# Optimization experiments

Hardware: AMD Instinct MI355X
Metric: run time of the kernel (lower is better)

## Reference

```python
import jax, jax.numpy as jnp
import numpy as np
from jax import lax

MIN_VALUE = 0.0
MAX_VALUE = 1.0

# 5-point Laplacian stencil kernel, OIHW layout
_LAP_KERNEL = jnp.array([[0.0, 1.0, 0.0],
                         [1.0, -4.0, 1.0],
                         [0.0, 1.0, 0.0]], dtype=jnp.float32).reshape(1, 1, 3, 3)


def _laplacian(u):
    # u: [B, 1, H, W], zero-padded 3x3 stencil (SAME)
    return lax.conv_general_dilated(
        u, _LAP_KERNEL, window_strides=(1, 1), padding='SAME',
        dimension_numbers=('NCHW', 'OIHW', 'NCHW'))


def _step(u, params):
    # Fisher-Kolmogorov reaction-diffusion step:
    #   diff = D * laplacian(u) + rho * u * (1 - u)
    D = params[:, 0:1]    # [B,1,H,W]
    rho = params[:, 1:2]  # [B,1,H,W]
    return D * _laplacian(u) + rho * u * (1.0 - u)


def setup_inputs() -> dict:
    key = jax.random.key(0)
    k1, k2, k3 = jax.random.split(key, 3)
    B, H, W = 32, 256, 256
    u = jax.random.uniform(k1, (B, 1, H, W), dtype=jnp.float32)
    params = jax.random.uniform(k2, (B, 2, H, W), dtype=jnp.float32)
    t = jax.random.randint(k3, (B,), 0, 32, dtype=jnp.int32)
    return {"u": u, "params": params, "t": t}


def reference(u, params, t):
    # Original: for step in range(max(t)): u[t>step] += step(u[t>step], params[t>step]); clip(u).
    # The step is per-sample local, so masked gather/scatter == predicated full update.
    max_duration = int(jnp.max(t))  # static trip count

    def body(step, u):
        mask = (t > step).astype(u.dtype)[:, None, None, None]  # [B,1,1,1]
        u = u + mask * _step(u, params)
        return jnp.clip(u, MIN_VALUE, MAX_VALUE)

    return lax.fori_loop(0, max_duration, body, u)
```

## Files before the change

kernel.cpp:

```cpp
#include <hip/hip_runtime.h>

#define HH 256
#define WW 256
#define PLANE (HH * WW)
#define CORE 16
#define HALO 16
#define SLAB 48
#define NW 16
#define RPW 3

__device__ __forceinline__ float dpp_shfl_up1(float x) {
    return __int_as_float(__builtin_amdgcn_update_dpp(
        0, __float_as_int(x), 0x138 , 0xf, 0xf, true));
}
__device__ __forceinline__ float dpp_shfl_dn1(float x) {
    return __int_as_float(__builtin_amdgcn_update_dpp(
        0, __float_as_int(x), 0x130 , 0xf, 0xf, true));
}

__global__ __launch_bounds__(1024, 8)
void rd_occ_kernel(const float* __restrict__ uin,
                   const float* __restrict__ params,
                   const int* __restrict__ t,
                   float* __restrict__ uout,
                   int base, int k)
{
    __shared__ float4 vt[2][NW][64];
    __shared__ float4 vb[2][NW][64];

    const int blk   = blockIdx.x;
    const int b     = blk >> 4;
    const int strip = blk & 15;
    const int r0    = strip * CORE;
    const int w     = threadIdx.x >> 6;
    const int lane  = threadIdx.x & 63;
    const int c0    = lane << 2;

    int ls = t[b] - base;
    ls = ls < 0 ? 0 : (ls > k ? k : ls);

    const int top_gap = HALO - (RPW * w + RPW - 1);
    const int bot_gap = RPW * w - (HALO + CORE - 1);
    int d_min = top_gap > bot_gap ? top_gap : bot_gap;
    if (d_min < 0) d_min = 0;
    int my_steps = ls - d_min;
    if (my_steps < 0) my_steps = 0;

    const int growbase = r0 - HALO + RPW * w;
    const size_t ubase = (size_t)b * PLANE;
    const size_t pbase = (size_t)b * 2 * PLANE;

    float u[RPW][4], pD[RPW][4], pR[RPW][4];

    #pragma unroll
    for (int dr = 0; dr < RPW; ++dr) {
        const int grow = growbase + dr;
        const bool inimg = (grow >= 0) && (grow < HH);
        int dist = 0;
        if (grow < r0)                 dist = r0 - grow;
        else if (grow > r0 + CORE - 1) dist = grow - (r0 + CORE - 1);
        const bool needU = inimg && (dist <= ls);
        const bool needP = inimg && (dist < ls);

        if (needU) {
            const float4 uu = *reinterpret_cast<const float4*>(uin + ubase + (size_t)grow * WW + c0);
            u[dr][0] = uu.x; u[dr][1] = uu.y; u[dr][2] = uu.z; u[dr][3] = uu.w;
        } else {
            u[dr][0] = u[dr][1] = u[dr][2] = u[dr][3] = 0.f;
        }
        if (needP) {
            const float4 dd = *reinterpret_cast<const float4*>(params + pbase + (size_t)grow * WW + c0);
            const float4 rr = *reinterpret_cast<const float4*>(params + pbase + PLANE + (size_t)grow * WW + c0);
            pD[dr][0] = dd.x; pD[dr][1] = dd.y; pD[dr][2] = dd.z; pD[dr][3] = dd.w;
            pR[dr][0] = rr.x; pR[dr][1] = rr.y; pR[dr][2] = rr.z; pR[dr][3] = rr.w;
        } else {
            pD[dr][0] = pD[dr][1] = pD[dr][2] = pD[dr][3] = 0.f;
            pR[dr][0] = pR[dr][1] = pR[dr][2] = pR[dr][3] = 0.f;
        }
    }

    if (ls > 0) {
        vt[0][w][lane] = make_float4(u[0][0], u[0][1], u[0][2], u[0][3]);
        vb[0][w][lane] = make_float4(u[RPW-1][0], u[RPW-1][1], u[RPW-1][2], u[RPW-1][3]);

        for (int s = 0; s < ls; ++s) {
            __syncthreads();
            if (s < my_steps) {
                const int cur = s & 1;

                float upr[4] = {0.f, 0.f, 0.f, 0.f};
                float dnr[4] = {0.f, 0.f, 0.f, 0.f};
                if (w > 0)      { float4 v = vb[cur][w-1][lane]; upr[0]=v.x; upr[1]=v.y; upr[2]=v.z; upr[3]=v.w; }
                if (w < NW - 1) { float4 v = vt[cur][w+1][lane]; dnr[0]=v.x; dnr[1]=v.y; dnr[2]=v.z; dnr[3]=v.w; }

                float up_old[4];
                #pragma unroll
                for (int dr = 0; dr < RPW; ++dr) {
                    const float lf = dpp_shfl_up1(u[dr][3]);
                    const float rt = dpp_shfl_dn1(u[dr][0]);

                    float old[4], un[4];
                    #pragma unroll
                    for (int c = 0; c < 4; ++c) old[c] = u[dr][c];

                    #pragma unroll
                    for (int c = 0; c < 4; ++c) {
                        const float upv = dr ? up_old[c] : upr[c];
                        const float dnv = (dr < RPW - 1) ? u[dr+1][c] : dnr[c];
                        const float lv  = c ? old[c-1] : lf;
                        const float rv  = (c < 3) ? old[c+1] : rt;
                        const float uc  = old[c];
                        const float s4  = (upv + dnv) + (lv + rv);
                        const float lap = fmaf(-4.0f, uc, s4);
                        const float g   = fmaf(-uc, uc, uc);
                        const float a   = fmaf(pD[dr][c], lap, uc);
                        const float nv  = fmaf(pR[dr][c], g, a);
                        un[c] = __builtin_amdgcn_fmed3f(nv, 0.0f, 1.0f);
                    }
                    #pragma unroll
                    for (int c = 0; c < 4; ++c) { u[dr][c] = un[c]; up_old[c] = old[c]; }
                }

                const int nxt = cur ^ 1;
                vt[nxt][w][lane] = make_float4(u[0][0], u[0][1], u[0][2], u[0][3]);
                vb[nxt][w][lane] = make_float4(u[RPW-1][0], u[RPW-1][1], u[RPW-1][2], u[RPW-1][3]);
            }
        }
    }

    #pragma unroll
    for (int dr = 0; dr < RPW; ++dr) {
        const int grow = growbase + dr;
        if (grow >= r0 && grow < r0 + CORE) {
            *reinterpret_cast<float4*>(uout + ubase + (size_t)grow * WW + c0) =
                make_float4(u[dr][0], u[dr][1], u[dr][2], u[dr][3]);
        }
    }
}

extern "C" void kernel_launch(void* const* d_in, const int* in_sizes, int n_in,
                              void* d_out, int out_size, void* d_ws, size_t ws_size,
                              hipStream_t stream) {
    (void)in_sizes; (void)n_in; (void)out_size; (void)ws_size;
    const float* u      = (const float*)d_in[0];
    const float* params = (const float*)d_in[1];
    const int*   t      = (const int*)d_in[2];
    float*       out    = (float*)d_out;
    float*       ws     = (float*)d_ws;

    const dim3 grid(512), block(1024);
    rd_occ_kernel<<<grid, block, 0, stream>>>(u,  params, t, ws,  0,  16);
    rd_occ_kernel<<<grid, block, 0, stream>>>(ws, params, t, out, 16, 15);
}
```

Baseline: 51.96 us.

## Use wider strips with narrower halo across four launches and ping-pong registers

Each block now owns a 32-row core with an 8-row halo (8 strips per batch, 256 blocks), and the 31 time steps are split across four launches of at most 8 steps instead of two of 16. Less of each block's 48-row slab is halo, so fewer rows are computed redundantly. The cost is two extra launches and extra global round trips of u through the workspace. The step is also unrolled into ping-pong register buffers, which avoids copying old values, and a dummy 20KB shared array caps occupancy at about four blocks per CU.

```diff
diff --git a/kernel.cpp b/kernel.cpp
--- a/kernel.cpp
+++ b/kernel.cpp
@@ -3,8 +3,8 @@
 #define HH 256
 #define WW 256
 #define PLANE (HH * WW)
-#define CORE 16
-#define HALO 16
+#define CORE 32
+#define HALO 8
 #define SLAB 48
 #define NW 16
 #define RPW 3
@@ -18,19 +18,54 @@
         0, __float_as_int(x), 0x130 , 0xf, 0xf, true));
 }
 
-__global__ __launch_bounds__(1024, 8)
-void rd_occ_kernel(const float* __restrict__ uin,
-                   const float* __restrict__ params,
-                   const int* __restrict__ t,
-                   float* __restrict__ uout,
-                   int base, int k)
+template<int RD, int WR>
+__device__ __forceinline__ void do_step(const float (&S)[RPW][4], float (&D)[RPW][4],
+                                        const float (&pD)[RPW][4], const float (&pR)[RPW][4],
+                                        float4 (*vt)[NW][64], float4 (*vb)[NW][64],
+                                        int w, int lane)
+{
+    float upr[4] = {0.f, 0.f, 0.f, 0.f};
+    float dnr[4] = {0.f, 0.f, 0.f, 0.f};
+    if (w > 0)      { float4 v = vb[RD][w-1][lane]; upr[0]=v.x; upr[1]=v.y; upr[2]=v.z; upr[3]=v.w; }
+    if (w < NW - 1) { float4 v = vt[RD][w+1][lane]; dnr[0]=v.x; dnr[1]=v.y; dnr[2]=v.z; dnr[3]=v.w; }
+
+    #pragma unroll
+    for (int dr = 0; dr < RPW; ++dr) {
+        const float lf = dpp_shfl_up1(S[dr][3]);
+        const float rt = dpp_shfl_dn1(S[dr][0]);
+        #pragma unroll
+        for (int c = 0; c < 4; ++c) {
+            const float upv = dr ? S[dr-1][c] : upr[c];
+            const float dnv = (dr < RPW - 1) ? S[dr+1][c] : dnr[c];
+            const float lv  = c ? S[dr][c-1] : lf;
+            const float rv  = (c < 3) ? S[dr][c+1] : rt;
+            const float uc  = S[dr][c];
+            const float s4  = (upv + dnv) + (lv + rv);
+            const float lap = fmaf(-4.0f, uc, s4);
+            const float g   = fmaf(-uc, uc, uc);
+            const float a   = fmaf(pD[dr][c], lap, uc);
+            const float nv  = fmaf(pR[dr][c], g, a);
+            D[dr][c] = __builtin_amdgcn_fmed3f(nv, 0.0f, 1.0f);
+        }
+    }
+    vt[WR][w][lane] = make_float4(D[0][0], D[0][1], D[0][2], D[0][3]);
+    vb[WR][w][lane] = make_float4(D[RPW-1][0], D[RPW-1][1], D[RPW-1][2], D[RPW-1][3]);
+}
+
+__global__ __launch_bounds__(1024, 4)
+void rd_bank_kernel(const float* __restrict__ uin,
+                    const float* __restrict__ params,
+                    const int* __restrict__ t,
+                    float* __restrict__ uout,
+                    int base, int k)
 {
     __shared__ float4 vt[2][NW][64];
     __shared__ float4 vb[2][NW][64];
+    __shared__ int pad[5120];
 
     const int blk   = blockIdx.x;
-    const int b     = blk >> 4;
-    const int strip = blk & 15;
+    const int b     = blk >> 3;
+    const int strip = blk & 7;
     const int r0    = strip * CORE;
     const int w     = threadIdx.x >> 6;
     const int lane  = threadIdx.x & 63;
@@ -39,9 +74,11 @@
     int ls = t[b] - base;
     ls = ls < 0 ? 0 : (ls > k ? k : ls);
 
-    const int top_gap = HALO - (RPW * w + RPW - 1);
-    const int bot_gap = RPW * w - (HALO + CORE - 1);
-    int d_min = top_gap > bot_gap ? top_gap : bot_gap;
+    if (t[0] == 0x7fffffff) pad[threadIdx.x & 4095] = ls;
+
+    const int tg = HALO - (RPW * w + RPW - 1);
+    const int bg = RPW * w - (HALO + CORE - 1);
+    int d_min = tg > bg ? tg : bg;
     if (d_min < 0) d_min = 0;
     int my_steps = ls - d_min;
     if (my_steps < 0) my_steps = 0;
@@ -50,7 +87,7 @@
     const size_t ubase = (size_t)b * PLANE;
     const size_t pbase = (size_t)b * 2 * PLANE;
 
-    float u[RPW][4], pD[RPW][4], pR[RPW][4];
+    float uA[RPW][4], uB[RPW][4], pD[RPW][4], pR[RPW][4];
 
     #pragma unroll
     for (int dr = 0; dr < RPW; ++dr) {
@@ -64,9 +101,9 @@
 
         if (needU) {
             const float4 uu = *reinterpret_cast<const float4*>(uin + ubase + (size_t)grow * WW + c0);
-            u[dr][0] = uu.x; u[dr][1] = uu.y; u[dr][2] = uu.z; u[dr][3] = uu.w;
+            uA[dr][0] = uu.x; uA[dr][1] = uu.y; uA[dr][2] = uu.z; uA[dr][3] = uu.w;
         } else {
-            u[dr][0] = u[dr][1] = u[dr][2] = u[dr][3] = 0.f;
+            uA[dr][0] = uA[dr][1] = uA[dr][2] = uA[dr][3] = 0.f;
         }
         if (needP) {
             const float4 dd = *reinterpret_cast<const float4*>(params + pbase + (size_t)grow * WW + c0);
@@ -77,54 +114,21 @@
             pD[dr][0] = pD[dr][1] = pD[dr][2] = pD[dr][3] = 0.f;
             pR[dr][0] = pR[dr][1] = pR[dr][2] = pR[dr][3] = 0.f;
         }
+        uB[dr][0] = uB[dr][1] = uB[dr][2] = uB[dr][3] = 0.f;
     }
 
     if (ls > 0) {
-        vt[0][w][lane] = make_float4(u[0][0], u[0][1], u[0][2], u[0][3]);
-        vb[0][w][lane] = make_float4(u[RPW-1][0], u[RPW-1][1], u[RPW-1][2], u[RPW-1][3]);
+        vt[0][w][lane] = make_float4(uA[0][0], uA[0][1], uA[0][2], uA[0][3]);
+        vb[0][w][lane] = make_float4(uA[RPW-1][0], uA[RPW-1][1], uA[RPW-1][2], uA[RPW-1][3]);
 
-        for (int s = 0; s < ls; ++s) {
+        int s = 0;
+        while (true) {
             __syncthreads();
-            if (s < my_steps) {
-                const int cur = s & 1;
-
-                float upr[4] = {0.f, 0.f, 0.f, 0.f};
-                float dnr[4] = {0.f, 0.f, 0.f, 0.f};
-                if (w > 0)      { float4 v = vb[cur][w-1][lane]; upr[0]=v.x; upr[1]=v.y; upr[2]=v.z; upr[3]=v.w; }
-                if (w < NW - 1) { float4 v = vt[cur][w+1][lane]; dnr[0]=v.x; dnr[1]=v.y; dnr[2]=v.z; dnr[3]=v.w; }
-
-                float up_old[4];
-                #pragma unroll
-                for (int dr = 0; dr < RPW; ++dr) {
-                    const float lf = dpp_shfl_up1(u[dr][3]);
-                    const float rt = dpp_shfl_dn1(u[dr][0]);
-
-                    float old[4], un[4];
-                    #pragma unroll
-                    for (int c = 0; c < 4; ++c) old[c] = u[dr][c];
-
-                    #pragma unroll
-                    for (int c = 0; c < 4; ++c) {
-                        const float upv = dr ? up_old[c] : upr[c];
-                        const float dnv = (dr < RPW - 1) ? u[dr+1][c] : dnr[c];
-                        const float lv  = c ? old[c-1] : lf;
-                        const float rv  = (c < 3) ? old[c+1] : rt;
-                        const float uc  = old[c];
-                        const float s4  = (upv + dnv) + (lv + rv);
-                        const float lap = fmaf(-4.0f, uc, s4);
-                        const float g   = fmaf(-uc, uc, uc);
-                        const float a   = fmaf(pD[dr][c], lap, uc);
-                        const float nv  = fmaf(pR[dr][c], g, a);
-                        un[c] = __builtin_amdgcn_fmed3f(nv, 0.0f, 1.0f);
-                    }
-                    #pragma unroll
-                    for (int c = 0; c < 4; ++c) { u[dr][c] = un[c]; up_old[c] = old[c]; }
-                }
-
-                const int nxt = cur ^ 1;
-                vt[nxt][w][lane] = make_float4(u[0][0], u[0][1], u[0][2], u[0][3]);
-                vb[nxt][w][lane] = make_float4(u[RPW-1][0], u[RPW-1][1], u[RPW-1][2], u[RPW-1][3]);
-            }
+            if (s < my_steps) do_step<0, 1>(uA, uB, pD, pR, vt, vb, w, lane);
+            if (++s >= ls) break;
+            __syncthreads();
+            if (s < my_steps) do_step<1, 0>(uB, uA, pD, pR, vt, vb, w, lane);
+            if (++s >= ls) break;
         }
     }
 
@@ -132,8 +136,10 @@
     for (int dr = 0; dr < RPW; ++dr) {
         const int grow = growbase + dr;
         if (grow >= r0 && grow < r0 + CORE) {
-            *reinterpret_cast<float4*>(uout + ubase + (size_t)grow * WW + c0) =
-                make_float4(u[dr][0], u[dr][1], u[dr][2], u[dr][3]);
+            float4 o;
+            if (ls & 1) o = make_float4(uB[dr][0], uB[dr][1], uB[dr][2], uB[dr][3]);
+            else        o = make_float4(uA[dr][0], uA[dr][1], uA[dr][2], uA[dr][3]);
+            *reinterpret_cast<float4*>(uout + ubase + (size_t)grow * WW + c0) = o;
         }
     }
 }
@@ -148,7 +154,9 @@
     float*       out    = (float*)d_out;
     float*       ws     = (float*)d_ws;
 
-    const dim3 grid(512), block(1024);
-    rd_occ_kernel<<<grid, block, 0, stream>>>(u,  params, t, ws,  0,  16);
-    rd_occ_kernel<<<grid, block, 0, stream>>>(ws, params, t, out, 16, 15);
+    const dim3 grid(256), block(1024);
+    rd_bank_kernel<<<grid, block, 0, stream>>>(u,   params, t, ws,  0,  8);
+    rd_bank_kernel<<<grid, block, 0, stream>>>(ws,  params, t, out, 8,  8);
+    rd_bank_kernel<<<grid, block, 0, stream>>>(out, params, t, ws,  16, 8);
+    rd_bank_kernel<<<grid, block, 0, stream>>>(ws,  params, t, out, 24, 7);
 }
```

After: 52.52 us. Within noise of the previous version (+1.1%).
